# Optimization experiments

Measured on AMD Instinct MI355X. Metric: run time of the kernel, lower is better.

## Reference

```python
import jax, jax.numpy as jnp
import numpy as np

B = 32768        # batch
S = 256          # subnet_num
H1, H2 = 10, 6   # subnet_arch
L2_SMOOTH = 1e-3
EPS = 1e-10


def setup_inputs() -> dict:
    key = jax.random.key(0)
    k = jax.random.split(key, 7)
    def glorot(kk, shape, fan_in, fan_out):
        return (jax.random.normal(kk, shape, jnp.float32)
                * np.float32(np.sqrt(2.0 / (fan_in + fan_out))))
    x = jax.random.normal(k[0], (B, S), jnp.float32)
    W1 = glorot(k[1], (S, 1, H1), 1, H1)
    b1 = jnp.zeros((S, H1), jnp.float32)
    W2 = glorot(k[2], (S, H1, H2), H1, H2)
    b2 = jnp.zeros((S, H2), jnp.float32)
    W3 = glorot(k[3], (S, H2, 1), H2, 1)
    b3 = jnp.zeros((S, 1), jnp.float32)
    return {"x": x, "W1": W1, "b1": b1, "W2": W2, "b2": b2, "W3": W3, "b3": b3}


def _mlp_scalar(xs, W1, b1, W2, b2, W3, b3):
    # xs: scalar input of one subnet for one sample
    h = jnp.tanh(xs * W1[0] + b1)   # [H1]
    h = jnp.tanh(h @ W2 + b2)       # [H2]
    return (h @ W3 + b3)[0]         # scalar


def _per_subnet(fn):
    # inner vmap over batch (x axis 0, params broadcast), outer over subnets
    inner = jax.vmap(fn, in_axes=(0, None, None, None, None, None, None))
    return jax.vmap(inner, in_axes=(1, 0, 0, 0, 0, 0, 0))  # -> [S, B]


def reference(x, W1, b1, W2, b2, W3, b3):
    out = _per_subnet(_mlp_scalar)(x, W1, b1, W2, b2, W3, b3)           # [S, B]
    d2f = jax.grad(jax.grad(_mlp_scalar))                               # Hessian diag (scalar input)
    g2 = _per_subnet(d2f)(x, W1, b1, W2, b2, W3, b3)                    # [S, B]
    # training-mode batch stats (population std, as tf.math.reduce_std)
    mean = jnp.mean(out, axis=1, keepdims=True)                         # [S, 1]
    std = jnp.maximum(jnp.std(out, axis=1, keepdims=True), EPS)         # [S, 1]
    out_bn = ((out - mean) / std).T                                     # [B, S]
    smooth_loss = L2_SMOOTH * jnp.sum(jnp.mean(g2 * g2, axis=1) / std[:, 0])
    return out_bn, smooth_loss
```

## Files before the change

kernel.cpp:

```cpp
#include <hip/hip_runtime.h>
#include <math.h>

#define B 32768
#define S 256
#define H1 10
#define H2 6
#define ROWS 512
#define CH (B / ROWS)
#define WPB 4
#define L2_SMOOTH 1e-3f
#define EPS 1e-10f

__device__ __forceinline__ int rfl_i(int x) { return __builtin_amdgcn_readfirstlane(x); }
__device__ __forceinline__ float rfl(float x) {
    return __int_as_float(__builtin_amdgcn_readfirstlane(__float_as_int(x)));
}

__device__ __forceinline__ void tanh_pair(float x, float& th, float& s2) {
    const float e = __builtin_amdgcn_exp2f(x * 2.885390081777927f);
    const float r = __builtin_amdgcn_rcpf(e + 1.0f);
    th = fmaf(-2.0f, r, 1.0f);
    s2 = (4.0f * r) * (1.0f - r);
}

__global__ __launch_bounds__(256, 6) void k1_mlp(
    const float* __restrict__ x,
    const float* __restrict__ W1, const float* __restrict__ b1,
    const float* __restrict__ W2, const float* __restrict__ b2,
    const float* __restrict__ W3, const float* __restrict__ b3,
    float* __restrict__ out,
    float* __restrict__ psum,
    float* __restrict__ psum2,
    float* __restrict__ pg2)
{
    const int t   = threadIdx.x;
    const int wid = blockIdx.x * WPB + rfl_i(t >> 6);
    const int l   = t & 63;
    const int s   = wid & (S - 1);
    const int c   = wid >> 8;

    float w1[H1], bb1[H1], m2w1[H1], w2s[H1][H2], bb2[H2], w3s[H2];
#pragma unroll
    for (int i = 0; i < H1; ++i) {
        w1[i]   = W1[s * H1 + i];
        bb1[i]  = b1[s * H1 + i];
        m2w1[i] = -2.0f * w1[i];
    }
#pragma unroll
    for (int i = 0; i < H1; ++i)
#pragma unroll
        for (int j = 0; j < H2; ++j) w2s[i][j] = rfl(W2[(s * H1 + i) * H2 + j]);
#pragma unroll
    for (int j = 0; j < H2; ++j) {
        bb2[j] = b2[s * H2 + j];
        asm("" : "+v"(bb2[j]));
        w3s[j] = rfl(W3[s * H2 + j]);
    }
    float bb3 = b3[s];
    asm("" : "+v"(bb3));

    const size_t base = (size_t)(c * ROWS) * S + s;
    const float* px = x   + base;
    float*       po = out + base;
    const int loff = l * S;

    float so = 0.0f, so2 = 0.0f, sg2 = 0.0f;

    for (int k = 0; k < ROWS / 64; ++k) {
        const float xs = px[k * 64 * S + loff];

        float v[H2], vp[H2], vpp[H2];
        {
            float h, tt;
            tanh_pair(fmaf(xs, w1[0], bb1[0]), h, tt);
            const float hp  = tt * w1[0];
            const float hpp = (h * hp) * m2w1[0];
#pragma unroll
            for (int j = 0; j < H2; ++j) {
                v[j]   = fmaf(h, w2s[0][j], bb2[j]);
                vp[j]  = hp  * w2s[0][j];
                vpp[j] = hpp * w2s[0][j];
            }
        }
#pragma unroll
        for (int i = 1; i < H1; ++i) {
            float h, tt;
            tanh_pair(fmaf(xs, w1[i], bb1[i]), h, tt);
            const float hp  = tt * w1[i];
            const float hpp = (h * hp) * m2w1[i];
#pragma unroll
            for (int j = 0; j < H2; ++j) {
                v[j]   = fmaf(h,   w2s[i][j], v[j]);
                vp[j]  = fmaf(hp,  w2s[i][j], vp[j]);
                vpp[j] = fmaf(hpp, w2s[i][j], vpp[j]);
            }
        }

        float o, g2;
        {
            float g, tg;
            tanh_pair(v[0], g, tg);
            const float c0  = -2.0f * (g * vp[0]);
            const float gpp = tg * fmaf(c0, vp[0], vpp[0]);
            o  = fmaf(g, w3s[0], bb3);
            g2 = gpp * w3s[0];
        }
#pragma unroll
        for (int j = 1; j < H2; ++j) {
            float g, tg;
            tanh_pair(v[j], g, tg);
            const float cj  = -2.0f * (g * vp[j]);
            const float gpp = tg * fmaf(cj, vp[j], vpp[j]);
            o  = fmaf(g,     w3s[j], o);
            g2 = fmaf(w3s[j], gpp,   g2);
        }

        po[k * 64 * S + loff] = o;
        so += o; so2 = fmaf(o, o, so2); sg2 = fmaf(g2, g2, sg2);
    }

#pragma unroll
    for (int m = 1; m < 64; m <<= 1) {
        so  += __shfl_xor(so,  m, 64);
        so2 += __shfl_xor(so2, m, 64);
        sg2 += __shfl_xor(sg2, m, 64);
    }
    if (l == 0) {
        psum [s * CH + c] = so;
        psum2[s * CH + c] = so2;
        pg2  [s * CH + c] = sg2;
    }
}

__global__ __launch_bounds__(64) void k2_reduce(
    const float* __restrict__ psum, const float* __restrict__ psum2,
    const float* __restrict__ pg2,
    float* __restrict__ mean_arr, float* __restrict__ rstd_arr,
    float* __restrict__ smooth_arr)
{
    const int s = blockIdx.x;
    const int l = threadIdx.x;

    float a  = psum [s * CH + l];
    float b_ = psum2[s * CH + l];
    float cc = pg2  [s * CH + l];
#pragma unroll
    for (int m = 1; m < 64; m <<= 1) {
        a  += __shfl_xor(a,  m, 64);
        b_ += __shfl_xor(b_, m, 64);
        cc += __shfl_xor(cc, m, 64);
    }
    if (l == 0) {
        const float inv_b = 1.0f / (float)B;
        const float mean  = a * inv_b;
        float var = b_ * inv_b - mean * mean;
        var = fmaxf(var, 0.0f);
        const float stdv = fmaxf(sqrtf(var), EPS);
        const float rstd = 1.0f / stdv;
        mean_arr[s]   = mean;
        rstd_arr[s]   = rstd;
        smooth_arr[s] = (cc * inv_b) * rstd;
    }
}

#define K3_NORM_BLOCKS (B * S / (256 * 4))
__global__ __launch_bounds__(256) void k3_norm(
    float* __restrict__ out,
    const float* __restrict__ mean_arr, const float* __restrict__ rstd_arr,
    const float* __restrict__ smooth_arr)
{
    if ((int)blockIdx.x == K3_NORM_BLOCKS) {
        const int t = threadIdx.x;
        __shared__ float sa[256];
        sa[t] = smooth_arr[t];
        __syncthreads();
        for (int st = 128; st > 0; st >>= 1) {
            if (t < st) sa[t] += sa[t + st];
            __syncthreads();
        }
        if (t == 0) out[B * S] = L2_SMOOTH * sa[0];
        return;
    }

    const int i4   = (int)blockIdx.x * 256 + (int)threadIdx.x;
    const int base = i4 * 4;
    float4 v = *reinterpret_cast<float4*>(&out[base]);
    const int s0 = base & (S - 1);
    v.x = (v.x - mean_arr[s0 + 0]) * rstd_arr[s0 + 0];
    v.y = (v.y - mean_arr[s0 + 1]) * rstd_arr[s0 + 1];
    v.z = (v.z - mean_arr[s0 + 2]) * rstd_arr[s0 + 2];
    v.w = (v.w - mean_arr[s0 + 3]) * rstd_arr[s0 + 3];
    *reinterpret_cast<float4*>(&out[base]) = v;
}

extern "C" void kernel_launch(void* const* d_in, const int* in_sizes, int n_in,
                              void* d_out, int out_size, void* d_ws, size_t ws_size,
                              hipStream_t stream) {
    const float* x  = (const float*)d_in[0];
    const float* W1 = (const float*)d_in[1];
    const float* b1 = (const float*)d_in[2];
    const float* W2 = (const float*)d_in[3];
    const float* b2 = (const float*)d_in[4];
    const float* W3 = (const float*)d_in[5];
    const float* b3 = (const float*)d_in[6];
    float* out = (float*)d_out;

    float* psum   = (float*)d_ws;
    float* psum2  = psum  + S * CH;
    float* pg2    = psum2 + S * CH;
    float* meanA  = pg2   + S * CH;
    float* rstdA  = meanA + S;
    float* smooth = rstdA + S;

    k1_mlp<<<S * CH / WPB, 64 * WPB, 0, stream>>>(
        x, W1, b1, W2, b2, W3, b3, out, psum, psum2, pg2);
    k2_reduce<<<S, 64, 0, stream>>>(psum, psum2, pg2, meanA, rstdA, smooth);
    k3_norm<<<K3_NORM_BLOCKS + 1, 256, 0, stream>>>(out, meanA, rstdA, smooth);
}
```

Before: 113.6 us.

## Pack layer-2 FMAs into float2 vectors, prescale weights, process two rows per iteration

Layer-2 weights and biases are pre-multiplied by 2/ln2 so the exp2 argument needs no extra multiply. The derivative constants are rescaled to match (w^2 in m2w1, ln2 and ln2/2 factors). The H2 accumulators become float2 vectors so the compiler can emit packed FMA instructions. Each wave now handles two samples per loop iteration for more ILP, and the block size and launch bounds change to 128 threads. Register pressure rises sharply, which with the lower occupancy hint risks latency stalls.

```diff
diff --git a/kernel.cpp b/kernel.cpp
--- a/kernel.cpp
+++ b/kernel.cpp
@@ -7,23 +7,29 @@
 #define H2 6
 #define ROWS 512
 #define CH (B / ROWS)
-#define WPB 4
+#define WPB 2
 #define L2_SMOOTH 1e-3f
 #define EPS 1e-10f
+
+#define LSC 2.8853900817779268f
+#define C2L 0.6931471805599453f
+#define RLS 0.34657359027997264f
+
+typedef __attribute__((ext_vector_type(2))) float v2f;
 
 __device__ __forceinline__ int rfl_i(int x) { return __builtin_amdgcn_readfirstlane(x); }
 __device__ __forceinline__ float rfl(float x) {
     return __int_as_float(__builtin_amdgcn_readfirstlane(__float_as_int(x)));
 }
 
-__device__ __forceinline__ void tanh_pair(float x, float& th, float& s2) {
-    const float e = __builtin_amdgcn_exp2f(x * 2.885390081777927f);
+__device__ __forceinline__ void tanh_pair_s(float a_s, float& th, float& s2) {
+    const float e = __builtin_amdgcn_exp2f(a_s);
     const float r = __builtin_amdgcn_rcpf(e + 1.0f);
     th = fmaf(-2.0f, r, 1.0f);
     s2 = (4.0f * r) * (1.0f - r);
 }
 
-__global__ __launch_bounds__(256, 6) void k1_mlp(
+__global__ __launch_bounds__(128, 2) void k1_mlp(
     const float* __restrict__ x,
     const float* __restrict__ W1, const float* __restrict__ b1,
     const float* __restrict__ W2, const float* __restrict__ b2,
@@ -39,84 +45,111 @@
     const int s   = wid & (S - 1);
     const int c   = wid >> 8;
 
-    float w1[H1], bb1[H1], m2w1[H1], w2s[H1][H2], bb2[H2], w3s[H2];
+    float w1[H1], w1e[H1], b1e[H1], m2w1[H1];
 #pragma unroll
     for (int i = 0; i < H1; ++i) {
-        w1[i]   = W1[s * H1 + i];
-        bb1[i]  = b1[s * H1 + i];
-        m2w1[i] = -2.0f * w1[i];
-    }
+        const float w = rfl(W1[s * H1 + i]);
+        w1[i]   = w;
+        w1e[i]  = w * LSC;
+        m2w1[i] = -2.0f * w * w;
+        b1e[i]  = rfl(b1[s * H1 + i]) * LSC;
+        asm("" : "+v"(b1e[i]));
+    }
+    v2f w2p[H1][3];
 #pragma unroll
     for (int i = 0; i < H1; ++i)
 #pragma unroll
-        for (int j = 0; j < H2; ++j) w2s[i][j] = rfl(W2[(s * H1 + i) * H2 + j]);
+        for (int jp = 0; jp < 3; ++jp) {
+            w2p[i][jp].x = rfl(W2[(s * H1 + i) * H2 + 2 * jp    ]) * LSC;
+            w2p[i][jp].y = rfl(W2[(s * H1 + i) * H2 + 2 * jp + 1]) * LSC;
+        }
+    v2f b2p[3];
+#pragma unroll
+    for (int jp = 0; jp < 3; ++jp) {
+        b2p[jp].x = rfl(b2[s * H2 + 2 * jp    ]) * LSC;
+        b2p[jp].y = rfl(b2[s * H2 + 2 * jp + 1]) * LSC;
+    }
+    float w3s[H2], w3g[H2];
 #pragma unroll
     for (int j = 0; j < H2; ++j) {
-        bb2[j] = b2[s * H2 + j];
-        asm("" : "+v"(bb2[j]));
-        w3s[j] = rfl(W3[s * H2 + j]);
+        const float w = rfl(W3[s * H2 + j]);
+        w3s[j] = w;
+        w3g[j] = w * RLS;
     }
     float bb3 = b3[s];
     asm("" : "+v"(bb3));
 
-    const size_t base = (size_t)(c * ROWS) * S + s;
+    const size_t base = (size_t)(c * ROWS) * S + s + (size_t)l * S;
     const float* px = x   + base;
     float*       po = out + base;
-    const int loff = l * S;
 
     float so = 0.0f, so2 = 0.0f, sg2 = 0.0f;
 
-    for (int k = 0; k < ROWS / 64; ++k) {
-        const float xs = px[k * 64 * S + loff];
-
-        float v[H2], vp[H2], vpp[H2];
+#pragma unroll 1
+    for (int k = 0; k < ROWS / 128; ++k) {
+        const float xA = px[(size_t)(k * 128)      * S];
+        const float xB = px[(size_t)(k * 128 + 64) * S];
+
+        v2f vA[3], vpA[3], vppA[3], vB[3], vpB[3], vppB[3];
+
+        float hA, tA, hB, tB;
         {
-            float h, tt;
-            tanh_pair(fmaf(xs, w1[0], bb1[0]), h, tt);
-            const float hp  = tt * w1[0];
-            const float hpp = (h * hp) * m2w1[0];
-#pragma unroll
-            for (int j = 0; j < H2; ++j) {
-                v[j]   = fmaf(h, w2s[0][j], bb2[j]);
-                vp[j]  = hp  * w2s[0][j];
-                vpp[j] = hpp * w2s[0][j];
+            tanh_pair_s(fmaf(xA, w1e[0], b1e[0]), hA, tA);
+            tanh_pair_s(fmaf(xB, w1e[0], b1e[0]), hB, tB);
+            const float hpA = tA * w1[0], hppA = (hA * hpA) * m2w1[0];
+            const float hpB = tB * w1[0], hppB = (hB * hpB) * m2w1[0];
+#pragma unroll
+            for (int jp = 0; jp < 3; ++jp) {
+                vA[jp]   = hA   * w2p[0][jp] + b2p[jp];
+                vpA[jp]  = hpA  * w2p[0][jp];
+                vppA[jp] = hppA * w2p[0][jp];
+                vB[jp]   = hB   * w2p[0][jp] + b2p[jp];
+                vpB[jp]  = hpB  * w2p[0][jp];
+                vppB[jp] = hppB * w2p[0][jp];
             }
         }
 #pragma unroll
         for (int i = 1; i < H1; ++i) {
-            float h, tt;
-            tanh_pair(fmaf(xs, w1[i], bb1[i]), h, tt);
-            const float hp  = tt * w1[i];
-            const float hpp = (h * hp) * m2w1[i];
-#pragma unroll
-            for (int j = 0; j < H2; ++j) {
-                v[j]   = fmaf(h,   w2s[i][j], v[j]);
-                vp[j]  = fmaf(hp,  w2s[i][j], vp[j]);
-                vpp[j] = fmaf(hpp, w2s[i][j], vpp[j]);
+            tanh_pair_s(fmaf(xA, w1e[i], b1e[i]), hA, tA);
+            tanh_pair_s(fmaf(xB, w1e[i], b1e[i]), hB, tB);
+            const float hpA = tA * w1[i], hppA = (hA * hpA) * m2w1[i];
+            const float hpB = tB * w1[i], hppB = (hB * hpB) * m2w1[i];
+#pragma unroll
+            for (int jp = 0; jp < 3; ++jp) {
+                vA[jp]   = hA   * w2p[i][jp] + vA[jp];
+                vpA[jp]  = hpA  * w2p[i][jp] + vpA[jp];
+                vppA[jp] = hppA * w2p[i][jp] + vppA[jp];
+                vB[jp]   = hB   * w2p[i][jp] + vB[jp];
+                vpB[jp]  = hpB  * w2p[i][jp] + vpB[jp];
+                vppB[jp] = hppB * w2p[i][jp] + vppB[jp];
             }
         }
 
-        float o, g2;
-        {
-            float g, tg;
-            tanh_pair(v[0], g, tg);
-            const float c0  = -2.0f * (g * vp[0]);
-            const float gpp = tg * fmaf(c0, vp[0], vpp[0]);
-            o  = fmaf(g, w3s[0], bb3);
-            g2 = gpp * w3s[0];
-        }
-#pragma unroll
-        for (int j = 1; j < H2; ++j) {
-            float g, tg;
-            tanh_pair(v[j], g, tg);
-            const float cj  = -2.0f * (g * vp[j]);
-            const float gpp = tg * fmaf(cj, vp[j], vpp[j]);
-            o  = fmaf(g,     w3s[j], o);
-            g2 = fmaf(w3s[j], gpp,   g2);
-        }
-
-        po[k * 64 * S + loff] = o;
-        so += o; so2 = fmaf(o, o, so2); sg2 = fmaf(g2, g2, sg2);
+        float oA = bb3, g2A = 0.0f, oB = bb3, g2B = 0.0f;
+#pragma unroll
+        for (int jp = 0; jp < 3; ++jp) {
+            {   float g, tg; tanh_pair_s(vA[jp].x, g, tg);
+                const float q = g * vpA[jp].x, cc = -C2L * q;
+                const float gpp = tg * fmaf(cc, vpA[jp].x, vppA[jp].x);
+                oA = fmaf(g, w3s[2*jp], oA); g2A = fmaf(w3g[2*jp], gpp, g2A); }
+            {   float g, tg; tanh_pair_s(vA[jp].y, g, tg);
+                const float q = g * vpA[jp].y, cc = -C2L * q;
+                const float gpp = tg * fmaf(cc, vpA[jp].y, vppA[jp].y);
+                oA = fmaf(g, w3s[2*jp+1], oA); g2A = fmaf(w3g[2*jp+1], gpp, g2A); }
+            {   float g, tg; tanh_pair_s(vB[jp].x, g, tg);
+                const float q = g * vpB[jp].x, cc = -C2L * q;
+                const float gpp = tg * fmaf(cc, vpB[jp].x, vppB[jp].x);
+                oB = fmaf(g, w3s[2*jp], oB); g2B = fmaf(w3g[2*jp], gpp, g2B); }
+            {   float g, tg; tanh_pair_s(vB[jp].y, g, tg);
+                const float q = g * vpB[jp].y, cc = -C2L * q;
+                const float gpp = tg * fmaf(cc, vpB[jp].y, vppB[jp].y);
+                oB = fmaf(g, w3s[2*jp+1], oB); g2B = fmaf(w3g[2*jp+1], gpp, g2B); }
+        }
+
+        po[(size_t)(k * 128)      * S] = oA;
+        po[(size_t)(k * 128 + 64) * S] = oB;
+        so += oA; so2 = fmaf(oA, oA, so2); sg2 = fmaf(g2A, g2A, sg2);
+        so += oB; so2 = fmaf(oB, oB, so2); sg2 = fmaf(g2B, g2B, sg2);
     }
 
 #pragma unroll
```

Result: slower. 122.6 us (+7.9%).
